# Optimization experiments

Hardware: AMD Instinct MI355X
Metric: run time of the kernel (lower is better)

The kernel has to match this reference:

```python
import jax, jax.numpy as jnp
from jax import lax
import numpy as np

L, B, D_IN, D_OUT, D_MLP = 64, 32, 512, 512, 128
WINDOWS = [1, 3]
FEATS = [256, 128]
C = sum(FEATS)  # 384
EPS = 1e-5


def _leaky(x):
    return jnp.where(x >= 0, x, 0.1 * x)


def setup_inputs() -> dict:
    key = jax.random.key(0)
    ks = jax.random.split(key, 16)
    s = lambda k, shp: (jax.random.normal(k, shp, jnp.float32) * 0.02)
    inp = {}
    inp["x"] = jax.random.normal(ks[0], (L, B, D_IN), jnp.float32)
    inp["xs_mask"] = jnp.ones((L, B), jnp.float32)
    # conv + batchnorm params per window
    inp["conv_w0"] = s(ks[1], (FEATS[0], 1, D_IN * WINDOWS[0]))
    inp["conv_b0"] = jnp.zeros((FEATS[0],), jnp.float32)
    inp["gamma0"] = jnp.ones((FEATS[0],), jnp.float32)
    inp["beta0"] = jnp.zeros((FEATS[0],), jnp.float32)
    inp["conv_w1"] = s(ks[2], (FEATS[1], 1, D_IN * WINDOWS[1]))
    inp["conv_b1"] = jnp.zeros((FEATS[1],), jnp.float32)
    inp["gamma1"] = jnp.ones((FEATS[1],), jnp.float32)
    inp["beta1"] = jnp.zeros((FEATS[1],), jnp.float32)
    inp["w0"] = s(ks[3], (2 * C, D_MLP)); inp["b0"] = jnp.zeros((D_MLP,), jnp.float32)
    inp["w1"] = s(ks[4], (D_MLP, D_MLP)); inp["b1"] = jnp.zeros((D_MLP,), jnp.float32)
    inp["w2"] = s(ks[5], (D_MLP, D_MLP)); inp["b2"] = jnp.zeros((D_MLP,), jnp.float32)
    inp["w3"] = s(ks[6], (D_MLP, D_MLP)); inp["b3"] = jnp.zeros((D_MLP,), jnp.float32)
    # output MLP: Linear(d_mlp->d_mlp), Linear(d_mlp->d_out)
    inp["w4"] = s(ks[7], (D_MLP, D_MLP)); inp["b4"] = jnp.zeros((D_MLP,), jnp.float32)
    inp["w5"] = s(ks[8], (D_MLP, D_OUT)); inp["b5"] = jnp.zeros((D_OUT,), jnp.float32)
    return inp


def reference(x, xs_mask, conv_w0, conv_b0, gamma0, beta0, conv_w1, conv_b1,
              gamma1, beta1, w0, b0, w1, b1, w2, b2, w3, b3, w4, b4, w5, b5):
    # x: (L, B, E)
    x = x * xs_mask[:, :, None]
    xf = jnp.transpose(x, (1, 0, 2)).reshape(B, 1, L * D_IN)  # (B, 1, L*E)

    # CNN front-end: Conv1d(stride=d_in) + BatchNorm1d (batch stats) + LeakyReLU
    feats = []
    for win, cw, cb, g, bt in [(WINDOWS[0], conv_w0, conv_b0, gamma0, beta0),
                               (WINDOWS[1], conv_w1, conv_b1, gamma1, beta1)]:
        pad = (win - 1) // 2 * D_IN
        y = lax.conv_general_dilated(xf, cw, window_strides=(D_IN,),
                                     padding=[(pad, pad)],
                                     dimension_numbers=("NCH", "OIH", "NCH"))
        y = y + cb[None, :, None]  # (B, C_k, L)
        m = y.mean(axis=(0, 2))
        v = y.var(axis=(0, 2))  # biased var, as torch BN training mode
        y = (y - m[None, :, None]) / jnp.sqrt(v[None, :, None] + EPS)
        y = y * g[None, :, None] + bt[None, :, None]
        feats.append(_leaky(y))
    h = jnp.concatenate(feats, axis=1)          # (B, C, L)
    h = jnp.transpose(h, (2, 0, 1))             # (L, B, C)
    h = h * xs_mask[:, :, None]

    # Graph propagation: pairwise concat + first linear, split over concat halves
    # cat([h_i, h_j]) @ w0 == h_i @ w0[:C] + h_j @ w0[C:]  (avoids (L,L,B,2C) tensor)
    a = jnp.einsum("lbc,cd->lbd", h, w0[:C])    # (L, B, d_mlp)
    bb = jnp.einsum("lbc,cd->lbd", h, w0[C:])   # (L, B, d_mlp)
    p = _leaky(a[:, None, :, :] + bb[None, :, :, :] + b0)  # (L, L, B, d_mlp)
    p = _leaky(p @ w1 + b1)
    p = _leaky(p @ w2 + b2)
    p = _leaky(p @ w3 + b3)
    p = p * xs_mask[:, None, :, None]
    p = p.mean(axis=1)                          # (L, B, d_mlp)

    out = _leaky(p @ w4 + b4)
    out = _leaky(out @ w5 + b5)                 # (L, B, d_out)
    return out * xs_mask[:, :, None]
```

## Files before the change

kernel.cpp:

```cpp
#include <hip/hip_runtime.h>


#define BB 32
#define CCH 384

__device__ __forceinline__ float leaky(float x) { return fmaxf(x, 0.1f * x); }

typedef _Float16 f16x8 __attribute__((ext_vector_type(8)));
typedef float f32x4 __attribute__((ext_vector_type(4)));

union F8 { uint4 q; f16x8 h; };
union H2 { _Float16 f[2]; uint32_t u; };

__device__ __forceinline__ void split2(float d0, float d1,
                                       uint32_t& hw, uint32_t& lw) {
  H2 h, l;
  h.f[0] = (_Float16)d0; h.f[1] = (_Float16)d1;
  l.f[0] = (_Float16)((d0 - (float)h.f[0]) * 2048.0f);
  l.f[1] = (_Float16)((d1 - (float)h.f[1]) * 2048.0f);
  hw = h.u; lw = l.u;
}

__global__ __launch_bounds__(256) void conv_kernel(
    const float* __restrict__ x, const float* __restrict__ mask,
    const float* __restrict__ cw0, const float* __restrict__ cw1,
    const float* __restrict__ w1, const float* __restrict__ w2,
    const float* __restrict__ w3,
    float* __restrict__ yG, float* __restrict__ Ssum, float* __restrict__ Ssq,
    uint32_t* __restrict__ wpk)
{
  int bx = blockIdx.x;
  int tid = threadIdx.x;
  if (bx >= 256) {
    int e = (bx - 256) * 256 + tid;
    int L = e >> 13;
    int r = e & 8191;
    int k2 = r >> 7, n = r & 127;
    int k = k2 * 2;
    const float* w = (L == 0) ? w1 : (L == 1) ? w2 : w3;
    uint32_t hw, lw;
    split2(w[k * 128 + n], w[(k + 1) * 128 + n], hw, lw);
    wpk[L * 8192 + n * 64 + k2] = hw;
    wpk[24576 + L * 8192 + n * 64 + k2] = lw;
    return;
  }

  __shared__ uint32_t Ah[64 * 68], Al[64 * 68];
  __shared__ uint32_t Bh[64 * 68], Bl[64 * 68];

  int wid = __builtin_amdgcn_readfirstlane(tid >> 6);
  int lane = tid & 63;
  int m16 = lane & 15, q = lane >> 4;

  if (bx < 128) {
    int nb = bx & 3, mb = bx >> 2;
    int n0 = nb * 64;
    int row0 = mb * 64;
    const float* wbase = cw0 + n0 * 512;
    int wm = wid & 1, wn2 = wid >> 1;

    f32x4 hi[2][2], cr[2][2];
#pragma unroll
    for (int a = 0; a < 2; ++a)
#pragma unroll
      for (int b = 0; b < 2; ++b) {
        hi[a][b] = (f32x4){0.f, 0.f, 0.f, 0.f};
        cr[a][b] = (f32x4){0.f, 0.f, 0.f, 0.f};
      }

#pragma unroll 1
    for (int ch = 0; ch < 4; ++ch) {
      int kg0 = ch * 128;
      __syncthreads();
#pragma unroll 1
      for (int it = 0; it < 4; ++it) {
        int idx = it * 256 + tid;
        int r = idx >> 4;
        int k8 = (idx & 15) * 8;
        float d[8];
        int rowg = row0 + r;
        {
          float mv = mask[rowg];
          const float* xp = x + rowg * 512 + kg0 + k8;
          float4 a0 = *(const float4*)xp;
          float4 a1 = *(const float4*)(xp + 4);
          d[0] = a0.x * mv; d[1] = a0.y * mv; d[2] = a0.z * mv; d[3] = a0.w * mv;
          d[4] = a1.x * mv; d[5] = a1.y * mv; d[6] = a1.z * mv; d[7] = a1.w * mv;
        }
        uint4 hq, lq;
        split2(d[0], d[1], hq.x, lq.x);
        split2(d[2], d[3], hq.y, lq.y);
        split2(d[4], d[5], hq.z, lq.z);
        split2(d[6], d[7], hq.w, lq.w);
        *(uint4*)&Ah[r * 68 + k8 / 2] = hq;
        *(uint4*)&Al[r * 68 + k8 / 2] = lq;
        const float* wp = wbase + r * 512 + kg0 + k8;
        float4 b0v = *(const float4*)wp;
        float4 b1v = *(const float4*)(wp + 4);
        split2(b0v.x, b0v.y, hq.x, lq.x);
        split2(b0v.z, b0v.w, hq.y, lq.y);
        split2(b1v.x, b1v.y, hq.z, lq.z);
        split2(b1v.z, b1v.w, hq.w, lq.w);
        *(uint4*)&Bh[r * 68 + k8 / 2] = hq;
        *(uint4*)&Bl[r * 68 + k8 / 2] = lq;
      }
      __syncthreads();
#pragma unroll
      for (int ks = 0; ks < 4; ++ks) {
        int koff = ks * 16 + q * 4;
        F8 bh[2], bl[2];
#pragma unroll
        for (int nt = 0; nt < 2; ++nt) {
          int br = wn2 * 32 + nt * 16 + m16;
          bh[nt].q = *(const uint4*)&Bh[br * 68 + koff];
          bl[nt].q = *(const uint4*)&Bl[br * 68 + koff];
        }
#pragma unroll
        for (int mt = 0; mt < 2; ++mt) {
          int ar = wm * 32 + mt * 16 + m16;
          F8 ah, al;
          ah.q = *(const uint4*)&Ah[ar * 68 + koff];
          al.q = *(const uint4*)&Al[ar * 68 + koff];
#pragma unroll
          for (int nt = 0; nt < 2; ++nt) {
            hi[mt][nt] = __builtin_amdgcn_mfma_f32_16x16x32_f16(
                ah.h, bh[nt].h, hi[mt][nt], 0, 0, 0);
            cr[mt][nt] = __builtin_amdgcn_mfma_f32_16x16x32_f16(
                ah.h, bl[nt].h, cr[mt][nt], 0, 0, 0);
            cr[mt][nt] = __builtin_amdgcn_mfma_f32_16x16x32_f16(
                al.h, bh[nt].h, cr[mt][nt], 0, 0, 0);
          }
        }
      }
    }

    float y[2][2][4];
#pragma unroll
    for (int mt = 0; mt < 2; ++mt)
#pragma unroll
      for (int nt = 0; nt < 2; ++nt)
#pragma unroll
        for (int rg = 0; rg < 4; ++rg)
          y[mt][nt][rg] = hi[mt][nt][rg] + cr[mt][nt][rg] * (1.0f / 2048.0f);

#pragma unroll
    for (int nt = 0; nt < 2; ++nt) {
      float s = 0.f, s2 = 0.f;
#pragma unroll
      for (int mt = 0; mt < 2; ++mt)
#pragma unroll
        for (int rg = 0; rg < 4; ++rg) {
          float v = y[mt][nt][rg];
          s += v; s2 += v * v;
        }
      s  += __shfl_xor(s, 16, 64);  s  += __shfl_xor(s, 32, 64);
      s2 += __shfl_xor(s2, 16, 64); s2 += __shfl_xor(s2, 32, 64);
      if (lane < 16) {
        int c = n0 + wn2 * 32 + nt * 16 + m16;
        atomicAdd(&Ssum[c], s);
        atomicAdd(&Ssq[c], s2);
      }
    }

    __syncthreads();
    float* Yl = (float*)Ah;
#pragma unroll
    for (int mt = 0; mt < 2; ++mt)
#pragma unroll
      for (int nt = 0; nt < 2; ++nt)
#pragma unroll
        for (int rg = 0; rg < 4; ++rg)
          Yl[(wn2 * 32 + nt * 16 + m16) * 68 + wm * 32 + mt * 16 + q * 4 + rg] =
              y[mt][nt][rg];
    __syncthreads();
    {
      int c = tid >> 2, seg = (tid & 3) * 16;
#pragma unroll
      for (int j = 0; j < 16; j += 4)
        *(float4*)&yG[(n0 + c) * 2048 + row0 + seg + j] =
            *(const float4*)&Yl[c * 68 + seg + j];
    }
    return;
  }

  {
    int t = bx - 128;
    int nb3 = t & 1, mb3 = t >> 1;
    int n0 = 256 + nb3 * 64;
    int row0 = mb3 * 32;
    const float* wbase = cw1 + (n0 - 256) * 1536;

    f32x4 hi3[2], cr3[2];
#pragma unroll
    for (int mt = 0; mt < 2; ++mt) {
      hi3[mt] = (f32x4){0.f, 0.f, 0.f, 0.f};
      cr3[mt] = (f32x4){0.f, 0.f, 0.f, 0.f};
    }

#pragma unroll 1
    for (int ch = 0; ch < 12; ++ch) {
      int kg0 = ch * 128;
      int tap = kg0 >> 9;
      int d0 = kg0 & 511;
      int shift = (tap - 1) * 32;
      __syncthreads();
#pragma unroll 1
      for (int it = 0; it < 6; ++it) {
        int idx = it * 256 + tid;
        if (idx < 512) {
          int r = idx >> 4;
          int k8 = (idx & 15) * 8;
          float d[8];
          int rowg = row0 + r + shift;
          if ((unsigned)rowg < 2048u) {
            float mv = mask[rowg];
            const float* xp = x + rowg * 512 + d0 + k8;
            float4 a0 = *(const float4*)xp;
            float4 a1 = *(const float4*)(xp + 4);
            d[0] = a0.x * mv; d[1] = a0.y * mv; d[2] = a0.z * mv; d[3] = a0.w * mv;
            d[4] = a1.x * mv; d[5] = a1.y * mv; d[6] = a1.z * mv; d[7] = a1.w * mv;
          } else {
#pragma unroll
            for (int t2 = 0; t2 < 8; ++t2) d[t2] = 0.f;
          }
          uint4 hq, lq;
          split2(d[0], d[1], hq.x, lq.x);
          split2(d[2], d[3], hq.y, lq.y);
          split2(d[4], d[5], hq.z, lq.z);
          split2(d[6], d[7], hq.w, lq.w);
          *(uint4*)&Ah[r * 68 + k8 / 2] = hq;
          *(uint4*)&Al[r * 68 + k8 / 2] = lq;
        } else {
          int idx2 = idx - 512;
          int r = idx2 >> 4;
          int k8 = (idx2 & 15) * 8;
          const float* wp = wbase + r * 1536 + kg0 + k8;
          float4 b0v = *(const float4*)wp;
          float4 b1v = *(const float4*)(wp + 4);
          uint4 hq, lq;
          split2(b0v.x, b0v.y, hq.x, lq.x);
          split2(b0v.z, b0v.w, hq.y, lq.y);
          split2(b1v.x, b1v.y, hq.z, lq.z);
          split2(b1v.z, b1v.w, hq.w, lq.w);
          *(uint4*)&Bh[r * 68 + k8 / 2] = hq;
          *(uint4*)&Bl[r * 68 + k8 / 2] = lq;
        }
      }
      __syncthreads();
#pragma unroll
      for (int ks = 0; ks < 4; ++ks) {
        int koff = ks * 16 + q * 4;
        F8 bh, bl;
        int br = wid * 16 + m16;
        bh.q = *(const uint4*)&Bh[br * 68 + koff];
        bl.q = *(const uint4*)&Bl[br * 68 + koff];
#pragma unroll
        for (int mt = 0; mt < 2; ++mt) {
          int ar = mt * 16 + m16;
          F8 ah, al;
          ah.q = *(const uint4*)&Ah[ar * 68 + koff];
          al.q = *(const uint4*)&Al[ar * 68 + koff];
          hi3[mt] = __builtin_amdgcn_mfma_f32_16x16x32_f16(
              ah.h, bh.h, hi3[mt], 0, 0, 0);
          cr3[mt] = __builtin_amdgcn_mfma_f32_16x16x32_f16(
              ah.h, bl.h, cr3[mt], 0, 0, 0);
          cr3[mt] = __builtin_amdgcn_mfma_f32_16x16x32_f16(
              al.h, bh.h, cr3[mt], 0, 0, 0);
        }
      }
    }

    float y3[2][4];
#pragma unroll
    for (int mt = 0; mt < 2; ++mt)
#pragma unroll
      for (int rg = 0; rg < 4; ++rg)
        y3[mt][rg] = hi3[mt][rg] + cr3[mt][rg] * (1.0f / 2048.0f);

    {
      float s = 0.f, s2 = 0.f;
#pragma unroll
      for (int mt = 0; mt < 2; ++mt)
#pragma unroll
        for (int rg = 0; rg < 4; ++rg) {
          float v = y3[mt][rg];
          s += v; s2 += v * v;
        }
      s  += __shfl_xor(s, 16, 64);  s  += __shfl_xor(s, 32, 64);
      s2 += __shfl_xor(s2, 16, 64); s2 += __shfl_xor(s2, 32, 64);
      if (lane < 16) {
        int c = n0 + wid * 16 + m16;
        atomicAdd(&Ssum[c], s);
        atomicAdd(&Ssq[c], s2);
      }
    }

    __syncthreads();
    float* Yl = (float*)Ah;
#pragma unroll
    for (int mt = 0; mt < 2; ++mt)
#pragma unroll
      for (int rg = 0; rg < 4; ++rg)
        Yl[(wid * 16 + m16) * 34 + mt * 16 + q * 4 + rg] = y3[mt][rg];
    __syncthreads();
    {
      int c = tid >> 2, seg = (tid & 3) * 8;
#pragma unroll
      for (int j = 0; j < 8; j += 4)
        *(float4*)&yG[(n0 + c) * 2048 + row0 + seg + j] =
            *(const float4*)&Yl[c * 34 + seg + j];
    }
  }
}

__global__ __launch_bounds__(256) void ab_kernel(
    const float* __restrict__ yG, const float* __restrict__ Ssum,
    const float* __restrict__ Ssq,
    const float* __restrict__ g0, const float* __restrict__ be0,
    const float* __restrict__ g1, const float* __restrict__ be1,
    const float* __restrict__ mask, const float* __restrict__ w0,
    float* __restrict__ a_arr, float* __restrict__ bb_arr)
{
  int bx = blockIdx.x;
  int tid = threadIdx.x;
  __shared__ float As[64 * 20];
  __shared__ float Ws[64 * 68];
  __shared__ float scs[384], shs[384];
  for (int c = tid; c < 384; c += 256) {
    float Sv = Ssum[c], S2v = Ssq[c];
    float mean = Sv * (1.f / 2048.f);
    float var  = S2v * (1.f / 2048.f) - mean * mean;
    float g  = (c < 256) ? g0[c] : g1[c - 256];
    float be = (c < 256) ? be0[c] : be1[c - 256];
    float sc = g / sqrtf(var + 1e-5f);
    scs[c] = sc;
    shs[c] = be - mean * sc;
  }
  __syncthreads();

  int rt = bx >> 2, ct = bx & 3;
  int row0 = rt * 16, n0 = ct * 64;
  int cth = tid >> 2;
  int srr4 = (tid & 3) * 4;
  int wn16 = (tid & 3) * 16;
  int r4 = (tid >> 6) * 4;
  int n1 = tid & 63;
  const float* wbase = (n0 < 128) ? (w0 + n0) : (w0 + CCH * 128 + (n0 - 128));
  float4 mv = *(const float4*)(mask + row0 + srr4);

  float acc[4] = {0.f, 0.f, 0.f, 0.f};
#pragma unroll 1
  for (int c0 = 0; c0 < 384; c0 += 64) {
    int c = c0 + cth;
    float4 yv = *(const float4*)(yG + c * 2048 + row0 + srr4);
    float sc = scs[c], sh = shs[c];
    float4 wv0 = *(const float4*)(wbase + c * 128 + wn16);
    float4 wv1 = *(const float4*)(wbase + c * 128 + wn16 + 4);
    float4 wv2 = *(const float4*)(wbase + c * 128 + wn16 + 8);
    float4 wv3 = *(const float4*)(wbase + c * 128 + wn16 + 12);
    __syncthreads();
    float4 hv;
    hv.x = leaky(fmaf(yv.x, sc, sh)) * mv.x;
    hv.y = leaky(fmaf(yv.y, sc, sh)) * mv.y;
    hv.z = leaky(fmaf(yv.z, sc, sh)) * mv.z;
    hv.w = leaky(fmaf(yv.w, sc, sh)) * mv.w;
    *(float4*)&As[cth * 20 + srr4] = hv;
    *(float4*)&Ws[cth * 68 + wn16]      = wv0;
    *(float4*)&Ws[cth * 68 + wn16 + 4]  = wv1;
    *(float4*)&Ws[cth * 68 + wn16 + 8]  = wv2;
    *(float4*)&Ws[cth * 68 + wn16 + 12] = wv3;
    __syncthreads();
#pragma unroll 16
    for (int cc = 0; cc < 64; ++cc) {
      float4 a = *(const float4*)&As[cc * 20 + r4];
      float w  = Ws[cc * 68 + n1];
      acc[0] = fmaf(a.x, w, acc[0]);
      acc[1] = fmaf(a.y, w, acc[1]);
      acc[2] = fmaf(a.z, w, acc[2]);
      acc[3] = fmaf(a.w, w, acc[3]);
    }
  }
  float* dst; int nd;
  if (n0 < 128) { dst = a_arr; nd = n0; } else { dst = bb_arr; nd = n0 - 128; }
#pragma unroll
  for (int ri = 0; ri < 4; ++ri)
    dst[(row0 + r4 + ri) * 128 + nd + n1] = acc[ri];
}

__global__ __launch_bounds__(512, 3) void pair_kernel(
    const float* __restrict__ a_arr, const float* __restrict__ bb_arr,
    const float* __restrict__ b0, const uint32_t* __restrict__ wpk,
    const float* __restrict__ b1, const float* __restrict__ b2,
    const float* __restrict__ b3,
    const float* __restrict__ w4, const float* __restrict__ b4,
    const float* __restrict__ w5, const float* __restrict__ b5,
    const float* __restrict__ mask, float* __restrict__ out)
{
  __shared__ uint32_t Ahs[64 * 68];
  __shared__ uint32_t Als[64 * 68];
  int i = blockIdx.x, b = blockIdx.y;
  int tid = threadIdx.x;
  int browp = i * BB + b;

  int wid = __builtin_amdgcn_readfirstlane(tid >> 6);
  int lane = tid & 63;
  int m16 = lane & 15, q = lane >> 4;
  int wn16 = wid * 16;
  int wrow = wn16 + m16;

  F8 Wh, Wl, Whn, Wln;
  {
    const uint32_t* W0h = wpk + wrow * 64 + q * 4;
    const uint32_t* W0l = wpk + 24576 + wrow * 64 + q * 4;
    Wh.q = *(const uint4*)W0h;
    Wl.q = *(const uint4*)W0l;
  }

  {
    int k8 = (tid & 15) * 8;
    const float* ap = a_arr + browp * 128 + k8;
    const float* zp = b0 + k8;
    float az[8];
#pragma unroll
    for (int t = 0; t < 8; t += 4) {
      float4 av = *(const float4*)(ap + t);
      float4 zv = *(const float4*)(zp + t);
      az[t + 0] = av.x + zv.x; az[t + 1] = av.y + zv.y;
      az[t + 2] = av.z + zv.z; az[t + 3] = av.w + zv.w;
    }
#pragma unroll
    for (int it = 0; it < 2; ++it) {
      int r = (it * 512 + tid) >> 4;
      const float* bbp = bb_arr + (r * BB + b) * 128 + k8;
      float d[8];
#pragma unroll
      for (int t = 0; t < 8; t += 4) {
        float4 bv = *(const float4*)(bbp + t);
        d[t + 0] = leaky(az[t + 0] + bv.x);
        d[t + 1] = leaky(az[t + 1] + bv.y);
        d[t + 2] = leaky(az[t + 2] + bv.z);
        d[t + 3] = leaky(az[t + 3] + bv.w);
      }
      uint4 hq, lq;
      split2(d[0], d[1], hq.x, lq.x);
      split2(d[2], d[3], hq.y, lq.y);
      split2(d[4], d[5], hq.z, lq.z);
      split2(d[6], d[7], hq.w, lq.w);
      *(uint4*)&Ahs[r * 68 + k8 / 2] = hq;
      *(uint4*)&Als[r * 68 + k8 / 2] = lq;
    }
  }
  __syncthreads();

  f32x4 hi[4], cr[4];

#pragma unroll 1
  for (int L = 0; L < 3; ++L) {
    const uint32_t* WhL = wpk + L * 8192;
    const uint32_t* WlL = wpk + 24576 + L * 8192;
    const float* Bv = (L == 0) ? b1 : (L == 1) ? b2 : b3;
#pragma unroll
    for (int mt = 0; mt < 4; ++mt) {
      hi[mt] = (f32x4){0.f, 0.f, 0.f, 0.f};
      cr[mt] = (f32x4){0.f, 0.f, 0.f, 0.f};
    }

#pragma unroll
    for (int ks = 0; ks < 4; ++ks) {
      int koff = ks * 16 + q * 4;
      if (ks < 3) {
        Whn.q = *(const uint4*)(WhL + wrow * 64 + koff + 16);
        Wln.q = *(const uint4*)(WlL + wrow * 64 + koff + 16);
      } else if (L < 2) {
        Whn.q = *(const uint4*)(WhL + 8192 + wrow * 64 + q * 4);
        Wln.q = *(const uint4*)(WlL + 8192 + wrow * 64 + q * 4);
      }
#pragma unroll
      for (int mt = 0; mt < 4; ++mt) {
        int arow = mt * 16 + m16;
        F8 Ah, Al;
        Ah.q = *(const uint4*)&Ahs[arow * 68 + koff];
        Al.q = *(const uint4*)&Als[arow * 68 + koff];
        hi[mt] = __builtin_amdgcn_mfma_f32_16x16x32_f16(
            Ah.h, Wh.h, hi[mt], 0, 0, 0);
        cr[mt] = __builtin_amdgcn_mfma_f32_16x16x32_f16(
            Ah.h, Wl.h, cr[mt], 0, 0, 0);
        cr[mt] = __builtin_amdgcn_mfma_f32_16x16x32_f16(
            Al.h, Wh.h, cr[mt], 0, 0, 0);
      }
      Wh = Whn; Wl = Wln;
    }

    float bias = Bv[wrow];

    if (L < 2) {
      __syncthreads();
      int par = lane & 1;
      int colw = (wn16 + (m16 & ~1)) >> 1;
#pragma unroll
      for (int mt = 0; mt < 4; ++mt) {
#pragma unroll
        for (int rg = 0; rg < 4; ++rg) {
          float d = leaky(hi[mt][rg] + cr[mt][rg] * (1.0f / 2048.0f) + bias);
          float dn = __shfl_xor(d, 1, 64);
          float de = par ? dn : d;
          float do_ = par ? d : dn;
          uint32_t hw, lw;
          split2(de, do_, hw, lw);
          int row = mt * 16 + q * 4 + rg;
          if (par) Als[row * 68 + colw] = lw;
          else     Ahs[row * 68 + colw] = hw;
        }
      }
      __syncthreads();
    } else {
      float s = 0.f;
#pragma unroll
      for (int mt = 0; mt < 4; ++mt)
#pragma unroll
        for (int rg = 0; rg < 4; ++rg)
          s += leaky(hi[mt][rg] + cr[mt][rg] * (1.0f / 2048.0f) + bias);
      s += __shfl_xor(s, 16, 64);
      s += __shfl_xor(s, 32, 64);
      float mfac = (1.0f / 64.0f) * mask[browp];
      __syncthreads();
      float* scratch = (float*)Ahs;
      float* Pm = scratch;
      float* Tp = scratch + 128;
      float* T4 = scratch + 640;
      if (lane < 16) Pm[wrow] = s * mfac;
      __syncthreads();
      {
        int k = tid & 127, chh = tid >> 7;
        const float* w4c = w4 + (chh * 32) * 128 + k;
        const float* pc = Pm + chh * 32;
        float t = 0.f;
#pragma unroll 8
        for (int c0 = 0; c0 < 32; c0 += 4) {
          float4 pv = *(const float4*)&pc[c0];
          t = fmaf(pv.x, w4c[(c0 + 0) * 128], t);
          t = fmaf(pv.y, w4c[(c0 + 1) * 128], t);
          t = fmaf(pv.z, w4c[(c0 + 2) * 128], t);
          t = fmaf(pv.w, w4c[(c0 + 3) * 128], t);
        }
        Tp[chh * 128 + k] = t;
      }
      __syncthreads();
      if (tid < 128)
        T4[tid] = leaky(Tp[tid] + Tp[128 + tid] + Tp[256 + tid] +
                        Tp[384 + tid] + b4[tid]);
      __syncthreads();
      {
        float o = b5[tid];
#pragma unroll 4
        for (int c0 = 0; c0 < 128; c0 += 4) {
          float4 tv = *(const float4*)&T4[c0];
          o = fmaf(tv.x, w5[(c0 + 0) * 512 + tid], o);
          o = fmaf(tv.y, w5[(c0 + 1) * 512 + tid], o);
          o = fmaf(tv.z, w5[(c0 + 2) * 512 + tid], o);
          o = fmaf(tv.w, w5[(c0 + 3) * 512 + tid], o);
        }
        out[browp * 512 + tid] = leaky(o) * mask[browp];
      }
    }
  }
}

extern "C" void kernel_launch(void* const* d_in, const int* in_sizes, int n_in,
                              void* d_out, int out_size, void* d_ws, size_t ws_size,
                              hipStream_t stream) {
  const float* x    = (const float*)d_in[0];
  const float* mask = (const float*)d_in[1];
  const float* cw0  = (const float*)d_in[2];
  const float* g0   = (const float*)d_in[4];
  const float* be0  = (const float*)d_in[5];
  const float* cw1  = (const float*)d_in[6];
  const float* g1   = (const float*)d_in[8];
  const float* be1  = (const float*)d_in[9];
  const float* w0   = (const float*)d_in[10];
  const float* b0   = (const float*)d_in[11];
  const float* w1   = (const float*)d_in[12];
  const float* b1   = (const float*)d_in[13];
  const float* w2   = (const float*)d_in[14];
  const float* b2   = (const float*)d_in[15];
  const float* w3   = (const float*)d_in[16];
  const float* b3   = (const float*)d_in[17];
  const float* w4   = (const float*)d_in[18];
  const float* b4   = (const float*)d_in[19];
  const float* w5   = (const float*)d_in[20];
  const float* b5   = (const float*)d_in[21];

  float* ws     = (float*)d_ws;
  float* Ssum   = ws;
  float* Ssq    = ws + 384;
  float* yG     = ws + 768;
  uint32_t* wpk = (uint32_t*)(ws + 787200);
  float* a_arr  = ws + 836352;
  float* bb_arr = ws + 1098496;
  float* outp   = (float*)d_out;

  hipMemsetAsync(Ssum, 0, 768 * sizeof(float), stream);
  conv_kernel<<<352, 256, 0, stream>>>(x, mask, cw0, cw1, w1, w2, w3,
                                       yG, Ssum, Ssq, wpk);
  ab_kernel<<<512, 256, 0, stream>>>(yG, Ssum, Ssq, g0, be0, g1, be1,
                                     mask, w0, a_arr, bb_arr);
  dim3 g5(64, 32);
  pair_kernel<<<g5, 512, 0, stream>>>(a_arr, bb_arr, b0, wpk, b1, b2, b3,
                                      w4, b4, w5, b5, mask, outp);
}
```

Before: 269.0 us.

## Persist pair blocks over 8 batches with double-buffered prefetch; split output MLP kernel

```diff
diff --git a/kernel.cpp b/kernel.cpp
--- a/kernel.cpp
+++ b/kernel.cpp
@@ -387,181 +387,225 @@
     dst[(row0 + r4 + ri) * 128 + nd + n1] = acc[ri];
 }
 
-__global__ __launch_bounds__(512, 3) void pair_kernel(
+__global__ __launch_bounds__(512) void pair_kernel(
     const float* __restrict__ a_arr, const float* __restrict__ bb_arr,
     const float* __restrict__ b0, const uint32_t* __restrict__ wpk,
     const float* __restrict__ b1, const float* __restrict__ b2,
-    const float* __restrict__ b3,
-    const float* __restrict__ w4, const float* __restrict__ b4,
-    const float* __restrict__ w5, const float* __restrict__ b5,
-    const float* __restrict__ mask, float* __restrict__ out)
+    const float* __restrict__ b3, const float* __restrict__ mask,
+    float* __restrict__ p_arr)
 {
-  __shared__ uint32_t Ahs[64 * 68];
-  __shared__ uint32_t Als[64 * 68];
-  int i = blockIdx.x, b = blockIdx.y;
+  __shared__ uint32_t AhsD[2][64 * 68];
+  __shared__ uint32_t AlsD[2][64 * 68];
+  __shared__ float Pm[128];
+  int i = blockIdx.x, bp = blockIdx.y;
   int tid = threadIdx.x;
-  int browp = i * BB + b;
-
   int wid = __builtin_amdgcn_readfirstlane(tid >> 6);
   int lane = tid & 63;
   int m16 = lane & 15, q = lane >> 4;
-  int wn16 = wid * 16;
-  int wrow = wn16 + m16;
+  int wn16 = wid * 16, wrow = wn16 + m16;
+  int k8 = (tid & 15) * 8;
+  int r0 = tid >> 4;
 
   F8 Wh, Wl, Whn, Wln;
-  {
-    const uint32_t* W0h = wpk + wrow * 64 + q * 4;
-    const uint32_t* W0l = wpk + 24576 + wrow * 64 + q * 4;
-    Wh.q = *(const uint4*)W0h;
-    Wl.q = *(const uint4*)W0l;
-  }
-
-  {
-    int k8 = (tid & 15) * 8;
-    const float* ap = a_arr + browp * 128 + k8;
-    const float* zp = b0 + k8;
-    float az[8];
-#pragma unroll
-    for (int t = 0; t < 8; t += 4) {
-      float4 av = *(const float4*)(ap + t);
-      float4 zv = *(const float4*)(zp + t);
-      az[t + 0] = av.x + zv.x; az[t + 1] = av.y + zv.y;
-      az[t + 2] = av.z + zv.z; az[t + 3] = av.w + zv.w;
-    }
+  Wh.q = *(const uint4*)(wpk + wrow * 64 + q * 4);
+  Wl.q = *(const uint4*)(wpk + 24576 + wrow * 64 + q * 4);
+
+  float zz[8];
+  *(float4*)&zz[0] = *(const float4*)(b0 + k8);
+  *(float4*)&zz[4] = *(const float4*)(b0 + k8 + 4);
+
+  int bbase = bp * 8;
+  int brow0 = i * BB + bbase;
+
+  float av[8], bv[2][8];
+  auto LOADB = [&](int bt) {
+    const float* ap = a_arr + (i * BB + bt) * 128 + k8;
+    *(float4*)&av[0] = *(const float4*)ap;
+    *(float4*)&av[4] = *(const float4*)(ap + 4);
 #pragma unroll
     for (int it = 0; it < 2; ++it) {
-      int r = (it * 512 + tid) >> 4;
-      const float* bbp = bb_arr + (r * BB + b) * 128 + k8;
+      int r = it * 32 + r0;
+      const float* bbp = bb_arr + (r * BB + bt) * 128 + k8;
+      *(float4*)&bv[it][0] = *(const float4*)bbp;
+      *(float4*)&bv[it][4] = *(const float4*)(bbp + 4);
+    }
+  };
+  auto WRITEB = [&](int buf) {
+    uint32_t* Ah = AhsD[buf];
+    uint32_t* Al = AlsD[buf];
+#pragma unroll
+    for (int it = 0; it < 2; ++it) {
+      int r = it * 32 + r0;
       float d[8];
 #pragma unroll
-      for (int t = 0; t < 8; t += 4) {
-        float4 bv = *(const float4*)(bbp + t);
-        d[t + 0] = leaky(az[t + 0] + bv.x);
-        d[t + 1] = leaky(az[t + 1] + bv.y);
-        d[t + 2] = leaky(az[t + 2] + bv.z);
-        d[t + 3] = leaky(az[t + 3] + bv.w);
-      }
+      for (int j = 0; j < 8; ++j) d[j] = leaky(av[j] + zz[j] + bv[it][j]);
       uint4 hq, lq;
       split2(d[0], d[1], hq.x, lq.x);
       split2(d[2], d[3], hq.y, lq.y);
       split2(d[4], d[5], hq.z, lq.z);
       split2(d[6], d[7], hq.w, lq.w);
-      *(uint4*)&Ahs[r * 68 + k8 / 2] = hq;
-      *(uint4*)&Als[r * 68 + k8 / 2] = lq;
-    }
-  }
+      *(uint4*)&Ah[r * 68 + k8 / 2] = hq;
+      *(uint4*)&Al[r * 68 + k8 / 2] = lq;
+    }
+  };
+
+  LOADB(bbase);
+  WRITEB(0);
   __syncthreads();
 
   f32x4 hi[4], cr[4];
 
 #pragma unroll 1
-  for (int L = 0; L < 3; ++L) {
-    const uint32_t* WhL = wpk + L * 8192;
-    const uint32_t* WlL = wpk + 24576 + L * 8192;
-    const float* Bv = (L == 0) ? b1 : (L == 1) ? b2 : b3;
-#pragma unroll
-    for (int mt = 0; mt < 4; ++mt) {
-      hi[mt] = (f32x4){0.f, 0.f, 0.f, 0.f};
-      cr[mt] = (f32x4){0.f, 0.f, 0.f, 0.f};
-    }
-
-#pragma unroll
-    for (int ks = 0; ks < 4; ++ks) {
-      int koff = ks * 16 + q * 4;
-      if (ks < 3) {
-        Whn.q = *(const uint4*)(WhL + wrow * 64 + koff + 16);
-        Wln.q = *(const uint4*)(WlL + wrow * 64 + koff + 16);
-      } else if (L < 2) {
-        Whn.q = *(const uint4*)(WhL + 8192 + wrow * 64 + q * 4);
-        Wln.q = *(const uint4*)(WlL + 8192 + wrow * 64 + q * 4);
-      }
+  for (int t = 0; t < 8; ++t) {
+    int browp = brow0 + t;
+    if (t < 7) LOADB(bbase + t + 1);
+    int cur = t & 1;
+    uint32_t* Ahs = AhsD[cur];
+    uint32_t* Als = AlsD[cur];
+
+#pragma unroll 1
+    for (int L = 0; L < 3; ++L) {
+      const uint32_t* WhL = wpk + L * 8192;
+      const uint32_t* WlL = wpk + 24576 + L * 8192;
+      const float* Bv = (L == 0) ? b1 : (L == 1) ? b2 : b3;
 #pragma unroll
       for (int mt = 0; mt < 4; ++mt) {
-        int arow = mt * 16 + m16;
-        F8 Ah, Al;
-        Ah.q = *(const uint4*)&Ahs[arow * 68 + koff];
-        Al.q = *(const uint4*)&Als[arow * 68 + koff];
-        hi[mt] = __builtin_amdgcn_mfma_f32_16x16x32_f16(
-            Ah.h, Wh.h, hi[mt], 0, 0, 0);
-        cr[mt] = __builtin_amdgcn_mfma_f32_16x16x32_f16(
-            Ah.h, Wl.h, cr[mt], 0, 0, 0);
-        cr[mt] = __builtin_amdgcn_mfma_f32_16x16x32_f16(
-            Al.h, Wh.h, cr[mt], 0, 0, 0);
-      }
-      Wh = Whn; Wl = Wln;
-    }
-
-    float bias = Bv[wrow];
-
-    if (L < 2) {
-      __syncthreads();
-      int par = lane & 1;
-      int colw = (wn16 + (m16 & ~1)) >> 1;
-#pragma unroll
-      for (int mt = 0; mt < 4; ++mt) {
-#pragma unroll
-        for (int rg = 0; rg < 4; ++rg) {
-          float d = leaky(hi[mt][rg] + cr[mt][rg] * (1.0f / 2048.0f) + bias);
-          float dn = __shfl_xor(d, 1, 64);
-          float de = par ? dn : d;
-          float do_ = par ? d : dn;
-          uint32_t hw, lw;
-          split2(de, do_, hw, lw);
-          int row = mt * 16 + q * 4 + rg;
-          if (par) Als[row * 68 + colw] = lw;
-          else     Ahs[row * 68 + colw] = hw;
-        }
-      }
-      __syncthreads();
-    } else {
-      float s = 0.f;
-#pragma unroll
-      for (int mt = 0; mt < 4; ++mt)
-#pragma unroll
-        for (int rg = 0; rg < 4; ++rg)
-          s += leaky(hi[mt][rg] + cr[mt][rg] * (1.0f / 2048.0f) + bias);
-      s += __shfl_xor(s, 16, 64);
-      s += __shfl_xor(s, 32, 64);
-      float mfac = (1.0f / 64.0f) * mask[browp];
-      __syncthreads();
-      float* scratch = (float*)Ahs;
-      float* Pm = scratch;
-      float* Tp = scratch + 128;
-      float* T4 = scratch + 640;
-      if (lane < 16) Pm[wrow] = s * mfac;
-      __syncthreads();
-      {
-        int k = tid & 127, chh = tid >> 7;
-        const float* w4c = w4 + (chh * 32) * 128 + k;
-        const float* pc = Pm + chh * 32;
-        float t = 0.f;
+        hi[mt] = (f32x4){0.f, 0.f, 0.f, 0.f};
+        cr[mt] = (f32x4){0.f, 0.f, 0.f, 0.f};
+      }
+
+#pragma unroll
+      for (int ks = 0; ks < 4; ++ks) {
+        int koff = ks * 16 + q * 4;
+        if (ks < 3) {
+          Whn.q = *(const uint4*)(WhL + wrow * 64 + koff + 16);
+          Wln.q = *(const uint4*)(WlL + wrow * 64 + koff + 16);
+        } else {
+          const uint32_t* nh = (L < 2) ? (WhL + 8192) : wpk;
+          const uint32_t* nl = (L < 2) ? (WlL + 8192) : (wpk + 24576);
+          Whn.q = *(const uint4*)(nh + wrow * 64 + q * 4);
+          Wln.q = *(const uint4*)(nl + wrow * 64 + q * 4);
+        }
+#pragma unroll
+        for (int mt = 0; mt < 4; ++mt) {
+          int arow = mt * 16 + m16;
+          F8 Ah, Al;
+          Ah.q = *(const uint4*)&Ahs[arow * 68 + koff];
+          Al.q = *(const uint4*)&Als[arow * 68 + koff];
+          hi[mt] = __builtin_amdgcn_mfma_f32_16x16x32_f16(
+              Ah.h, Wh.h, hi[mt], 0, 0, 0);
+          cr[mt] = __builtin_amdgcn_mfma_f32_16x16x32_f16(
+              Ah.h, Wl.h, cr[mt], 0, 0, 0);
+          cr[mt] = __builtin_amdgcn_mfma_f32_16x16x32_f16(
+              Al.h, Wh.h, cr[mt], 0, 0, 0);
+        }
+        Wh = Whn; Wl = Wln;
+      }
+
+      float bias = Bv[wrow];
+
+      if (L < 2) {
+        __syncthreads();
+        int par = lane & 1;
+        int colw = (wn16 + (m16 & ~1)) >> 1;
+#pragma unroll
+        for (int mt = 0; mt < 4; ++mt) {
+#pragma unroll
+          for (int rg = 0; rg < 4; ++rg) {
+            float dd = leaky(hi[mt][rg] + cr[mt][rg] * (1.0f / 2048.0f) + bias);
+            float dn = __shfl_xor(dd, 1, 64);
+            float de = par ? dn : dd;
+            float do_ = par ? dd : dn;
+            uint32_t hw, lw;
+            split2(de, do_, hw, lw);
+            int row = mt * 16 + q * 4 + rg;
+            if (par) Als[row * 68 + colw] = lw;
+            else     Ahs[row * 68 + colw] = hw;
+          }
+        }
+        __syncthreads();
+        if (L == 0 && t < 7) WRITEB(cur ^ 1);
+      } else {
+        float s = 0.f;
+#pragma unroll
+        for (int mt = 0; mt < 4; ++mt)
+#pragma unroll
+          for (int rg = 0; rg < 4; ++rg)
+            s += leaky(hi[mt][rg] + cr[mt][rg] * (1.0f / 2048.0f) + bias);
+        s += __shfl_xor(s, 16, 64);
+        s += __shfl_xor(s, 32, 64);
+        float mfac = (1.0f / 64.0f) * mask[browp];
+        __syncthreads();
+        if (lane < 16) Pm[wrow] = s * mfac;
+        __syncthreads();
+        if (tid < 128) p_arr[browp * 128 + tid] = Pm[tid];
+      }
+    }
+  }
+}
+
+__global__ __launch_bounds__(256) void out_kernel(
+    const float* __restrict__ p_arr,
+    const float* __restrict__ w4, const float* __restrict__ b4,
+    const float* __restrict__ w5, const float* __restrict__ b5,
+    const float* __restrict__ mask, float* __restrict__ out)
+{
+  __shared__ float Ps[8 * 128];
+  __shared__ float Ts[8 * 128];
+  int bx = blockIdx.x;
+  int tid = threadIdx.x;
+  int row0 = bx * 8;
+
+  {
+    int o = tid * 4;
+    *(float4*)&Ps[o] = *(const float4*)(p_arr + row0 * 128 + o);
+  }
+  __syncthreads();
+
+  {
+    int o = tid * 4;
+    int rr = o >> 7, cc = o & 127;
+    float4 acc = *(const float4*)(b4 + cc);
+    const float* pr = Ps + rr * 128;
 #pragma unroll 8
-        for (int c0 = 0; c0 < 32; c0 += 4) {
-          float4 pv = *(const float4*)&pc[c0];
-          t = fmaf(pv.x, w4c[(c0 + 0) * 128], t);
-          t = fmaf(pv.y, w4c[(c0 + 1) * 128], t);
-          t = fmaf(pv.z, w4c[(c0 + 2) * 128], t);
-          t = fmaf(pv.w, w4c[(c0 + 3) * 128], t);
-        }
-        Tp[chh * 128 + k] = t;
-      }
-      __syncthreads();
-      if (tid < 128)
-        T4[tid] = leaky(Tp[tid] + Tp[128 + tid] + Tp[256 + tid] +
-                        Tp[384 + tid] + b4[tid]);
-      __syncthreads();
-      {
-        float o = b5[tid];
+    for (int c = 0; c < 128; ++c) {
+      float pv = pr[c];
+      float4 wv = *(const float4*)(w4 + c * 128 + cc);
+      acc.x = fmaf(pv, wv.x, acc.x);
+      acc.y = fmaf(pv, wv.y, acc.y);
+      acc.z = fmaf(pv, wv.z, acc.z);
+      acc.w = fmaf(pv, wv.w, acc.w);
+    }
+    float4 tv;
+    tv.x = leaky(acc.x); tv.y = leaky(acc.y);
+    tv.z = leaky(acc.z); tv.w = leaky(acc.w);
+    *(float4*)&Ts[o] = tv;
+  }
+  __syncthreads();
+
+  {
+    int kk = tid * 2;
+    float acc[8][2];
+    float b5v0 = b5[kk], b5v1 = b5[kk + 1];
+#pragma unroll
+    for (int r = 0; r < 8; ++r) { acc[r][0] = b5v0; acc[r][1] = b5v1; }
 #pragma unroll 4
-        for (int c0 = 0; c0 < 128; c0 += 4) {
-          float4 tv = *(const float4*)&T4[c0];
-          o = fmaf(tv.x, w5[(c0 + 0) * 512 + tid], o);
-          o = fmaf(tv.y, w5[(c0 + 1) * 512 + tid], o);
-          o = fmaf(tv.z, w5[(c0 + 2) * 512 + tid], o);
-          o = fmaf(tv.w, w5[(c0 + 3) * 512 + tid], o);
-        }
-        out[browp * 512 + tid] = leaky(o) * mask[browp];
-      }
+    for (int c = 0; c < 128; ++c) {
+      float2 wv = *(const float2*)(w5 + c * 512 + kk);
+#pragma unroll
+      for (int r = 0; r < 8; ++r) {
+        float tv = Ts[r * 128 + c];
+        acc[r][0] = fmaf(tv, wv.x, acc[r][0]);
+        acc[r][1] = fmaf(tv, wv.y, acc[r][1]);
+      }
+    }
+#pragma unroll
+    for (int r = 0; r < 8; ++r) {
+      float mk = mask[row0 + r];
+      float2 ov;
+      ov.x = leaky(acc[r][0]) * mk;
+      ov.y = leaky(acc[r][1]) * mk;
+      *(float2*)&out[(row0 + r) * 512 + kk] = ov;
     }
   }
 }
@@ -597,6 +641,7 @@
   uint32_t* wpk = (uint32_t*)(ws + 787200);
   float* a_arr  = ws + 836352;
   float* bb_arr = ws + 1098496;
+  float* p_arr  = yG;
   float* outp   = (float*)d_out;
 
   hipMemsetAsync(Ssum, 0, 768 * sizeof(float), stream);
@@ -604,7 +649,8 @@
                                        yG, Ssum, Ssq, wpk);
   ab_kernel<<<512, 256, 0, stream>>>(yG, Ssum, Ssq, g0, be0, g1, be1,
                                      mask, w0, a_arr, bb_arr);
-  dim3 g5(64, 32);
+  dim3 g5(64, 4);
   pair_kernel<<<g5, 512, 0, stream>>>(a_arr, bb_arr, b0, wpk, b1, b2, b3,
-                                      w4, b4, w5, b5, mask, outp);
+                                      mask, p_arr);
+  out_kernel<<<256, 256, 0, stream>>>(p_arr, w4, b4, w5, b5, mask, outp);
 }
```

Result: no change. 266.0 us (-1.1%).
